# Performance work log

Measured on AMD Instinct MI355X. Metric: run time of the kernel, lower is better.

Reference implementation:

```python
import jax, jax.numpy as jnp
import numpy as np

# StyleLossDiag: diag(gram(x)) vs precomputed target diag, MSE loss.
# diag(F @ F.T) == sum(F**2, axis=1), so we never materialize the
# (a*b)x(a*b) Gram matrix -- same math, O(n) instead of O(n^2 d).

A, B, C, D = 16, 512, 64, 64  # target_feature_shape


def gram_diag(x):
    a, b, c, d = x.shape
    feats = x.reshape(a * b, c * d)
    # diagonal of (feats @ feats.T) / (a*b*c*d)
    return jnp.sum(feats * feats, axis=1) / (a * b * c * d)


def setup_inputs() -> dict:
    key = jax.random.key(0)
    k1, k2 = jax.random.split(key)
    x = jax.random.normal(k1, (A, B, C, D), dtype=jnp.float32)
    # target buffer: diag(gram(target_feature)).detach() from __init__
    target_feature = jax.random.normal(k2, (A, B, C, D), dtype=jnp.float32)
    target = gram_diag(target_feature)  # shape [A*B] = [8192]
    return {"x": x, "target": target}


def reference(x, target):
    g = gram_diag(x)                      # [a*b]
    loss = jnp.mean((g - target) ** 2)    # F.mse_loss default 'mean'
    return loss
```

## Files before the change

### kernel.cpp

```cpp
#include <hip/hip_runtime.h>


#define ROWS     8192
#define ROWLEN   4096
#define INV_NORM (1.0f / 33554432.0f)

__global__ __launch_bounds__(256) void rowdiag_wave_kernel(
    const float* __restrict__ x,
    const float* __restrict__ target,
    float* __restrict__ ws)
{
    const int wave = threadIdx.x >> 6;
    const int lane = threadIdx.x & 63;
    const int row  = blockIdx.x * 4 + wave;

    const float4* xr = reinterpret_cast<const float4*>(x) + (size_t)row * (ROWLEN / 4);

    float a0 = 0.f, a1 = 0.f, a2 = 0.f, a3 = 0.f;
#pragma unroll
    for (int i = 0; i < 4; ++i) {
        float4 v0 = xr[lane + (4 * i + 0) * 64];
        float4 v1 = xr[lane + (4 * i + 1) * 64];
        float4 v2 = xr[lane + (4 * i + 2) * 64];
        float4 v3 = xr[lane + (4 * i + 3) * 64];
        a0 += v0.x * v0.x + v0.y * v0.y + v0.z * v0.z + v0.w * v0.w;
        a1 += v1.x * v1.x + v1.y * v1.y + v1.z * v1.z + v1.w * v1.w;
        a2 += v2.x * v2.x + v2.y * v2.y + v2.z * v2.z + v2.w * v2.w;
        a3 += v3.x * v3.x + v3.y * v3.y + v3.z * v3.z + v3.w * v3.w;
    }
    float s = (a0 + a1) + (a2 + a3);

#pragma unroll
    for (int off = 32; off > 0; off >>= 1)
        s += __shfl_down(s, off, 64);

    if (lane == 0) {
        float d = s * INV_NORM - target[row];
        ws[row] = d * d;
    }
}

__global__ __launch_bounds__(256) void final_reduce_kernel(
    const float* __restrict__ ws,
    float* __restrict__ out)
{
    const float4* w4 = reinterpret_cast<const float4*>(ws);
    float s = 0.f;
#pragma unroll
    for (int i = 0; i < ROWS / 4 / 256; ++i) {
        float4 v = w4[threadIdx.x + i * 256];
        s += (v.x + v.y) + (v.z + v.w);
    }

#pragma unroll
    for (int off = 32; off > 0; off >>= 1)
        s += __shfl_down(s, off, 64);

    __shared__ float lds[4];
    const int lane = threadIdx.x & 63;
    const int wave = threadIdx.x >> 6;
    if (lane == 0) lds[wave] = s;
    __syncthreads();

    if (threadIdx.x == 0)
        out[0] = ((lds[0] + lds[1]) + (lds[2] + lds[3])) * (1.0f / (float)ROWS);
}

extern "C" void kernel_launch(void* const* d_in, const int* in_sizes, int n_in,
                              void* d_out, int out_size, void* d_ws, size_t ws_size,
                              hipStream_t stream)
{
    const float* x      = (const float*)d_in[0];
    const float* target = (const float*)d_in[1];
    float* out = (float*)d_out;
    float* ws  = (float*)d_ws;

    rowdiag_wave_kernel<<<ROWS / 4, 256, 0, stream>>>(x, target, ws);
    final_reduce_kernel<<<1, 256, 0, stream>>>(ws, out);
}
```

Before: 26.90 us.

## Fuse row reduction and final reduce into one kernel with last-block spin gather

Merges the per-row squared-norm kernel and the final reduction kernel into a single launch with 1024-thread blocks, each covering 16 rows. Each block reduces its rows in shared memory and publishes a partial to the workspace with an atomic exchange. The last block polls the slots until they are non-negative, resets them to -1, and tree-reduces the values. This removes the second kernel launch and the per-row workspace round trip. The gather depends on the workspace starting at -1 (the first call may read stale data) and on the other blocks finishing while the last block spins, with only a bounded guard protecting against hangs.

```diff
diff --git a/kernel.cpp b/kernel.cpp
--- a/kernel.cpp
+++ b/kernel.cpp
@@ -3,16 +3,20 @@
 
 #define ROWS     8192
 #define ROWLEN   4096
+#define NBLK     512
+#define TPB      1024
 #define INV_NORM (1.0f / 33554432.0f)
 
-__global__ __launch_bounds__(256) void rowdiag_wave_kernel(
+__global__ __launch_bounds__(TPB) void styleloss_onekernel(
     const float* __restrict__ x,
     const float* __restrict__ target,
-    float* __restrict__ ws)
+    float* ws,
+    float* __restrict__ out)
 {
     const int wave = threadIdx.x >> 6;
     const int lane = threadIdx.x & 63;
-    const int row  = blockIdx.x * 4 + wave;
+    const int b    = blockIdx.x;
+    const int row  = b * 16 + wave;
 
     const float4* xr = reinterpret_cast<const float4*>(x) + (size_t)row * (ROWLEN / 4);
 
@@ -34,36 +38,49 @@
     for (int off = 32; off > 0; off >>= 1)
         s += __shfl_down(s, off, 64);
 
+    __shared__ float wsum[16];
+    __shared__ float vals[NBLK];
     if (lane == 0) {
         float d = s * INV_NORM - target[row];
-        ws[row] = d * d;
+        wsum[wave] = d * d;
     }
-}
+    __syncthreads();
 
-__global__ __launch_bounds__(256) void final_reduce_kernel(
-    const float* __restrict__ ws,
-    float* __restrict__ out)
-{
-    const float4* w4 = reinterpret_cast<const float4*>(ws);
-    float s = 0.f;
+    if (threadIdx.x == 0) {
+        float P = 0.f;
 #pragma unroll
-    for (int i = 0; i < ROWS / 4 / 256; ++i) {
-        float4 v = w4[threadIdx.x + i * 256];
-        s += (v.x + v.y) + (v.z + v.w);
+        for (int i = 0; i < 16; ++i)
+            P += wsum[i];
+        atomicExch(&ws[b], P);
     }
 
+    if (b == NBLK - 1) {
+        const int t = threadIdx.x;
+        if (t < NBLK) {
+            float v;
+            int guard = 0;
+            while ((v = atomicAdd(&ws[t], 0.0f)) < 0.0f && guard < (1 << 20)) {
+                ++guard;
+                __builtin_amdgcn_s_sleep(2);
+            }
+            atomicExch(&ws[t], -1.0f);
+            vals[t] = v;
+        }
+        __syncthreads();
+
+        if (t < 256) vals[t] += vals[t + 256];
+        __syncthreads();
+        if (t < 128) vals[t] += vals[t + 128];
+        __syncthreads();
+        if (t < 64) {
+            float u = vals[t] + vals[t + 64];
 #pragma unroll
-    for (int off = 32; off > 0; off >>= 1)
-        s += __shfl_down(s, off, 64);
-
-    __shared__ float lds[4];
-    const int lane = threadIdx.x & 63;
-    const int wave = threadIdx.x >> 6;
-    if (lane == 0) lds[wave] = s;
-    __syncthreads();
-
-    if (threadIdx.x == 0)
-        out[0] = ((lds[0] + lds[1]) + (lds[2] + lds[3])) * (1.0f / (float)ROWS);
+            for (int off = 32; off > 0; off >>= 1)
+                u += __shfl_down(u, off, 64);
+            if (t == 0)
+                out[0] = u * (1.0f / (float)ROWS);
+        }
+    }
 }
 
 extern "C" void kernel_launch(void* const* d_in, const int* in_sizes, int n_in,
@@ -75,6 +92,5 @@
     float* out = (float*)d_out;
     float* ws  = (float*)d_ws;
 
-    rowdiag_wave_kernel<<<ROWS / 4, 256, 0, stream>>>(x, target, ws);
-    final_reduce_kernel<<<1, 256, 0, stream>>>(ws, out);
+    styleloss_onekernel<<<NBLK, TPB, 0, stream>>>(x, target, ws, out);
 }
```

Result: slower. 27.44 us (+2.0%).
